# Optimization experiments

Measured on AMD Instinct MI355X. Metric: run time of the kernel, lower is better.

## Reference

```python
import jax, jax.numpy as jnp
from jax import lax
import numpy as np

B = 2; C = 128; H = 128; W = 128; NPIX = H * W
HTH = 184; HTW = 180; NBINS = HTH * HTW
NSPH = 16384; KHT = 8; KSPH = 16
N0, N1, N2 = 1024, 256, 64
K0, K1, K2 = 8, 8, 8
EPS = 1e-5


def setup_inputs() -> dict:
    key = jax.random.key(0)
    ks = jax.random.split(key, 24)
    f32 = jnp.float32
    inp = {}
    inp["image"] = jax.random.normal(ks[0], (B, C, H, W), f32)
    inp["bn_gamma"] = jnp.ones((C,), f32)
    inp["bn_beta"] = jnp.zeros((C,), f32)
    inp["ht_idx"] = jax.random.randint(ks[1], (NBINS, KHT), 0, NPIX, jnp.int32)
    inp["ht_w"] = jax.random.uniform(ks[2], (NBINS, KHT), f32)
    inp["w_htconv"] = jax.random.normal(ks[3], (3, 3, C, C), f32) / np.sqrt(9.0 * C)
    inp["htbn_gamma"] = jnp.ones((C,), f32)
    inp["htbn_beta"] = jnp.zeros((C,), f32)
    inp["sph_idx"] = jax.random.randint(ks[4], (NSPH, KSPH), 0, NBINS, jnp.int32)
    inp["sph_w"] = jax.random.uniform(ks[5], (NSPH, KSPH), f32)
    inp["w_sc"] = jax.random.normal(ks[6], (3, 64, C), f32) / np.sqrt(1.0 * C)
    inp["b_sc"] = jnp.zeros((3, 64), f32)
    inp["scbn_gamma"] = jnp.ones((3, 64), f32)
    inp["scbn_beta"] = jnp.zeros((3, 64), f32)
    inp["dgcn_w"] = jax.random.normal(ks[7], (3, 4, 128, 64), f32) / np.sqrt(128.0)
    inp["dgcn_b"] = jnp.zeros((3, 4, 64), f32)
    inp["dgcn_hw"] = jax.random.normal(ks[8], (3, 64), f32) / 8.0
    inp["dgcn_hb"] = jnp.zeros((3,), f32)
    inp["ind0"] = jax.random.randint(ks[9], (B, N0), 0, NSPH, jnp.int32)
    inp["ind1"] = jax.random.randint(ks[10], (B, 3, N1), 0, NSPH, jnp.int32)
    inp["ind2"] = jax.random.randint(ks[11], (B, 3, N2), 0, NSPH, jnp.int32)
    # kNN-style edges: structured centers (each node repeated k times), random neighbors
    c0 = jnp.tile(jnp.repeat(jnp.arange(N0, dtype=jnp.int32), K0)[None], (B, 1))
    inp["edge0"] = jnp.stack([c0, jax.random.randint(ks[12], (B, N0 * K0), 0, N0, jnp.int32)], 1)
    c1 = jnp.broadcast_to(jnp.repeat(jnp.arange(N1, dtype=jnp.int32), K1)[None, None], (B, 3, N1 * K1))
    inp["edge1"] = jnp.stack([c1, jax.random.randint(ks[13], (B, 3, N1 * K1), 0, N1, jnp.int32)], 2)
    c2 = jnp.broadcast_to(jnp.repeat(jnp.arange(N2, dtype=jnp.int32), K2)[None, None], (B, 3, N2 * K2))
    inp["edge2"] = jnp.stack([c2, jax.random.randint(ks[14], (B, 3, N2 * K2), 0, N2, jnp.int32)], 2)
    inp["target0"] = jax.random.randint(ks[15], (B, N0), 0, 2, jnp.int32)
    inp["target1"] = jax.random.randint(ks[16], (B * 3, N1), 0, 2, jnp.int32)
    inp["target2"] = jax.random.randint(ks[17], (B * 3, N2), 0, 2, jnp.int32)
    return inp


def _bn2d(x, g, b):
    m = x.mean((0, 2, 3), keepdims=True)
    v = x.var((0, 2, 3), keepdims=True)
    return g[None, :, None, None] * (x - m) * lax.rsqrt(v + EPS) + b[None, :, None, None]


def _sphere(x_htf, sph_idx, sph_w, ind):
    # x_htf: [B,C,NBINS]; ind: [B,S] -> weighted gather of HT bins per sphere node
    mi = sph_idx[ind]          # [B,S,K]
    mw = sph_w[ind]            # [B,S,K]
    g = jax.vmap(lambda xb, ib: xb[:, ib])(x_htf, mi)   # [B,C,S,K]
    return (g * mw[:, None]).sum(-1)                    # [B,C,S]


def _sconv(x, w, b, g, be):
    # 1x1 conv [B,C,S]->[B,64,S] + BN1d (batch stats) + ReLU
    y = jnp.einsum('oc,bcs->bos', w, x) + b[None, :, None]
    m = y.mean((0, 2), keepdims=True)
    v = y.var((0, 2), keepdims=True)
    return jax.nn.relu(g[None, :, None] * (y - m) * lax.rsqrt(v + EPS) + be[None, :, None])


def _dgcn(x, edge, ws, bs, hw, hb, n, k):
    # x: [Bg,n,64]; edge: [Bg,2,n*k] (row0=center, row1=neighbor); 4 EdgeConv layers
    for i in range(4):
        xc = jnp.take_along_axis(x, edge[:, 0, :, None], axis=1)   # [Bg,n*k,Cin]
        xn = jnp.take_along_axis(x, edge[:, 1, :, None], axis=1)
        h = jax.nn.relu(jnp.concatenate([xc, xn - xc], -1) @ ws[i] + bs[i])
        x = h.reshape(x.shape[0], n, k, -1).max(2)                 # max over neighbors
    return x @ hw + hb                                             # [Bg,n] logits


def _bce(logits, target):
    t = target.astype(logits.dtype)
    l = jnp.maximum(logits, 0.0) - logits * t + jnp.log1p(jnp.exp(-jnp.abs(logits)))
    pos = t > 0.5
    npos = jnp.maximum(pos.sum(), 1).astype(l.dtype)
    nneg = jnp.maximum((~pos).sum(), 1).astype(l.dtype)
    return jnp.where(pos, l, 0.0).sum() / npos, jnp.where(pos, 0.0, l).sum() / nneg


def _forward(image, bn_gamma, bn_beta, ht_idx, ht_w, w_htconv, htbn_gamma, htbn_beta,
             sph_idx, sph_w, w_sc, b_sc, scbn_gamma, scbn_beta,
             dgcn_w, dgcn_b, dgcn_hw, dgcn_hb,
             ind0, ind1, ind2, edge0, edge1, edge2, target0, target1, target2):
    x = jax.nn.relu(_bn2d(image, bn_gamma, bn_beta))
    xf = x.reshape(B, C, NPIX)
    # Hough voting: each HT bin accumulates KHT weighted pixels
    ht = (xf[:, :, ht_idx] * ht_w).sum(-1).reshape(B, C, HTH, HTW)
    hc = lax.conv_general_dilated(ht, w_htconv, (1, 1), 'SAME',
                                  dimension_numbers=('NCHW', 'HWIO', 'NCHW'))
    x_htf = jax.nn.relu(_bn2d(hc, htbn_gamma, htbn_beta)).reshape(B, C, NBINS)

    # scale 0
    x0 = _sconv(_sphere(x_htf, sph_idx, sph_w, ind0),
                w_sc[0], b_sc[0], scbn_gamma[0], scbn_beta[0]).transpose(0, 2, 1)
    x0 = _dgcn(x0, edge0, dgcn_w[0], dgcn_b[0], dgcn_hw[0], dgcn_hb[0], N0, K0)   # [B,N0]
    # scale 1 (3 vanishing-point branches folded into batch)
    x1 = _sconv(_sphere(x_htf, sph_idx, sph_w, ind1.reshape(B, -1)),
                w_sc[1], b_sc[1], scbn_gamma[1], scbn_beta[1]).transpose(0, 2, 1)
    x1 = _dgcn(x1.reshape(B * 3, N1, 64), edge1.reshape(B * 3, 2, N1 * K1),
               dgcn_w[1], dgcn_b[1], dgcn_hw[1], dgcn_hb[1], N1, K1)              # [B*3,N1]
    # scale 2
    x2 = _sconv(_sphere(x_htf, sph_idx, sph_w, ind2.reshape(B, -1)),
                w_sc[2], b_sc[2], scbn_gamma[2], scbn_beta[2]).transpose(0, 2, 1)
    x2 = _dgcn(x2.reshape(B * 3, N2, 64), edge2.reshape(B * 3, 2, N2 * K2),
               dgcn_w[2], dgcn_b[2], dgcn_hw[2], dgcn_hb[2], N2, K2)              # [B*3,N2]

    lp0, ln0 = _bce(x0, target0)
    lp1, ln1 = _bce(x1, target1)
    lp2, ln2 = _bce(x2, target2)
    losses = jnp.stack([lp0, ln0, lp1, ln1, lp2, ln2])
    preds = jnp.concatenate([jax.nn.sigmoid(x0).reshape(B, -1),
                             jax.nn.sigmoid(x1).reshape(B, -1),
                             jax.nn.sigmoid(x2).reshape(B, -1)], axis=1)
    return losses, preds


def reference(image, bn_gamma, bn_beta, ht_idx, ht_w, w_htconv, htbn_gamma, htbn_beta,
              sph_idx, sph_w, w_sc, b_sc, scbn_gamma, scbn_beta,
              dgcn_w, dgcn_b, dgcn_hw, dgcn_hb,
              ind0, ind1, ind2, edge0, edge1, edge2, target0, target1, target2):
    return _forward(image, bn_gamma, bn_beta, ht_idx, ht_w, w_htconv, htbn_gamma, htbn_beta,
                    sph_idx, sph_w, w_sc, b_sc, scbn_gamma, scbn_beta,
                    dgcn_w, dgcn_b, dgcn_hw, dgcn_hb,
                    ind0, ind1, ind2, edge0, edge1, edge2, target0, target1, target2)
```

## Files before the change

### kernel.cpp

```cpp
#include <hip/hip_runtime.h>
#include <math.h>

#define B_ 2
#define C_ 128
#define NPIX_ 16384
#define HTH_ 184
#define HTW_ 180
#define NBINS_ 33120
#define PH_ 186
#define PW_ 184
#define NPB_ 1984
#define TOTN_ 3968
#define EPS_ 1e-5f

#define ST_HC_SUM 0
#define ST_HC_SQ  128
#define ST_SC_SUM 256
#define ST_SC_SQ  448
#define ST_LOSS   640
#define ST_IMG_A  704
#define ST_IMG_D  832
#define ST_IMG_S1 1472
#define ST_IMG_S2 1600

typedef __attribute__((ext_vector_type(8))) short v8s;
typedef __attribute__((ext_vector_type(4))) float v4f;

__device__ inline unsigned short f2b(float f) {
  unsigned u = __builtin_bit_cast(unsigned, f);
  unsigned r = u + 0x7fffu + ((u >> 16) & 1u);
  return (unsigned short)(r >> 16);
}
__device__ inline float b2f(unsigned short u) {
  unsigned v = ((unsigned)u) << 16;
  return __builtin_bit_cast(float, v);
}

__global__ void kw_weights(const float* __restrict__ w, const float* __restrict__ dw,
                           unsigned short* __restrict__ wtb, unsigned short* __restrict__ dwb) {
  int i = blockIdx.x*256 + threadIdx.x;
  if (i < 147456) {
    int tap = i >> 14, z = i & 16383;
    int j = z & 7, lane = (z >> 3) & 63, nt = (z >> 9) & 7, kt = (z >> 12) & 3;
    int l = lane & 15, q = lane >> 4;
    int co = nt*16 + l, ci = kt*32 + q*8 + j;
    wtb[i] = f2b(w[(tap*C_ + ci)*C_ + co]);
  } else {
    int i2 = i - 147456;
    int sl = i2 >> 13, z = i2 & 8191;
    int j = z & 7, lane = (z >> 3) & 63, nt = (z >> 9) & 3, kt = (z >> 11) & 3;
    int l = lane & 15, q = lane >> 4;
    int co = nt*16 + l, cc = kt*32 + q*8 + j;
    dwb[i2] = f2b(dw[(sl*128 + cc)*64 + co]);
  }
}

__global__ void k1_img_stats(const float* __restrict__ img, float* __restrict__ st) {
  int c = blockIdx.x; int chunk = blockIdx.y; int tid = threadIdx.x;
  float s1 = 0.f, s2 = 0.f;
  for (int i = chunk*4096 + tid; i < (chunk+1)*4096; i += 256) {
    int b = i >> 14, p = i & (NPIX_-1);
    float v = img[((size_t)(b*C_ + c))*NPIX_ + p];
    s1 += v; s2 += v*v;
  }
  __shared__ float r1[256], r2[256];
  r1[tid] = s1; r2[tid] = s2; __syncthreads();
  for (int off = 128; off; off >>= 1) {
    if (tid < off) { r1[tid] += r1[tid+off]; r2[tid] += r2[tid+off]; }
    __syncthreads();
  }
  if (tid == 0) {
    atomicAdd(&st[ST_IMG_S1 + c], r1[0]);
    atomicAdd(&st[ST_IMG_S2 + c], r2[0]);
  }
}
__global__ void k1b_fin(const float* __restrict__ g, const float* __restrict__ be,
                        float* __restrict__ st) {
  int c = threadIdx.x;
  float n = (float)(B_*NPIX_);
  float m = st[ST_IMG_S1+c]/n;
  float var = st[ST_IMG_S2+c]/n - m*m;
  float a = g[c]*rsqrtf(var + EPS_);
  st[ST_IMG_A+c] = a; st[ST_IMG_D+c] = be[c] - a*m;
}

__global__ void k2_bnrelu_t(const float* __restrict__ img, const float* __restrict__ st,
                            unsigned short* __restrict__ xt) {
  __shared__ float tile[32*65];
  int p0 = blockIdx.x*64, c0 = blockIdx.y*32, b = blockIdx.z;
  int tid = threadIdx.x;
  for (int r = 0; r < 8; r++) {
    int flat = tid + r*256;
    int row = flat >> 6, col = flat & 63;
    int c = c0 + row;
    float v = img[((size_t)(b*C_ + c))*NPIX_ + p0 + col];
    tile[row*65 + col] = fmaxf(st[ST_IMG_A + c]*v + st[ST_IMG_D + c], 0.f);
  }
  __syncthreads();
  for (int r = 0; r < 4; r++) {
    int flat = (tid + r*256)*2;
    int pl = flat >> 5, cl = flat & 31;
    unsigned lo = f2b(tile[cl*65 + pl]);
    unsigned hi = f2b(tile[(cl+1)*65 + pl]);
    *(unsigned*)&xt[((size_t)b*NPIX_ + p0 + pl)*C_ + c0 + cl] = lo | (hi << 16);
  }
}

__global__ void k3z_border(unsigned* __restrict__ htb2) {
  int i = blockIdx.x*256 + threadIdx.x;
  int d = i & 63;
  int cell = i >> 6;
  int b = cell / 1112, j = cell % 1112;
  int y, x;
  if (j < 184) { y = 0; x = j; }
  else if (j < 368) { y = 185; x = j - 184; }
  else { int c = j - 368; int xi = c / 186; y = c % 186; x = xi == 0 ? 0 : 180 + xi; }
  htb2[((size_t)(b*PH_ + y)*PW_ + x)*64 + d] = 0u;
}

__global__ void k3_hough(const unsigned* __restrict__ xt2, const int* __restrict__ hidx,
                         const float* __restrict__ hwt, unsigned* __restrict__ htb2) {
  int tid = threadIdx.x;
  int bin = blockIdx.x*4 + (tid >> 6);
  int b = blockIdx.y;
  int lane = tid & 63;
  const unsigned* base = xt2 + (size_t)b*NPIX_*64 + lane;
  float acc0 = 0.f, acc1 = 0.f;
  #pragma unroll
  for (int k = 0; k < 8; k++) {
    int p = hidx[bin*8 + k];
    float w = hwt[bin*8 + k];
    unsigned dv = base[(size_t)p*64];
    acc0 += w * b2f((unsigned short)(dv & 0xffff));
    acc1 += w * b2f((unsigned short)(dv >> 16));
  }
  int y = bin / HTW_, x = bin - y*HTW_;
  unsigned lo = f2b(acc0), hi = f2b(acc1);
  htb2[((size_t)(b*PH_ + y + 1)*PW_ + (x+1))*64 + lane] = lo | (hi << 16);
}

__global__ __launch_bounds__(256) void k4_mfma(
    const unsigned short* __restrict__ htb, const unsigned short* __restrict__ wtb,
    unsigned short* __restrict__ hcb, float* __restrict__ st) {
  __shared__ float red[1152];
  int tid = threadIdx.x;
  int w = tid >> 6, lane = tid & 63;
  int quad = lane >> 4, l16 = lane & 15;
  int ph = w & 1, ch = w >> 1;
  int b = blockIdx.y;
  int p0 = blockIdx.x*128 + ph*64;
  size_t ab[4];
  #pragma unroll
  for (int t = 0; t < 4; t++) {
    int px = p0 + t*16 + l16; if (px > NBINS_-1) px = NBINS_-1;
    int y = px / HTW_, x = px % HTW_;
    ab[t] = (((size_t)(b*PH_ + y))*PW_ + x)*C_ + quad*8;
  }
  v4f acc[4][4];
  #pragma unroll
  for (int t = 0; t < 4; t++)
    #pragma unroll
    for (int nt = 0; nt < 4; nt++) acc[t][nt] = (v4f){0,0,0,0};

  const v8s* wbase = (const v8s*)wtb + lane;
  #pragma unroll
  for (int tap = 0; tap < 9; tap++) {
    int dy = tap/3, dx = tap - dy*3;
    int toff = (dy*PW_ + dx)*C_;
    #pragma unroll
    for (int kt = 0; kt < 4; kt++) {
      v8s a[4];
      #pragma unroll
      for (int t = 0; t < 4; t++) a[t] = *(const v8s*)&htb[ab[t] + toff + kt*32];
      #pragma unroll
      for (int nt = 0; nt < 4; nt++) {
        v8s bf = wbase[(((tap*4 + kt)*8) + ch*4 + nt)*64];
        #pragma unroll
        for (int t = 0; t < 4; t++)
          acc[t][nt] = __builtin_amdgcn_mfma_f32_16x16x32_bf16(a[t], bf, acc[t][nt], 0, 0, 0);
      }
    }
  }
  float s1[4] = {0,0,0,0}, s2[4] = {0,0,0,0};
  #pragma unroll
  for (int t = 0; t < 4; t++) {
    #pragma unroll
    for (int nt = 0; nt < 4; nt++) {
      int co = ch*64 + nt*16 + l16;
      #pragma unroll
      for (int reg = 0; reg < 4; reg++) {
        int po = p0 + t*16 + quad*4 + reg;
        if (po < NBINS_) {
          float v = acc[t][nt][reg];
          hcb[((size_t)b*NBINS_ + po)*C_ + co] = f2b(v);
          s1[nt] += v; s2[nt] += v*v;
        }
      }
    }
  }
  int slot = ph*4 + quad;
  #pragma unroll
  for (int nt = 0; nt < 4; nt++) red[(ch*64 + nt*16 + l16)*9 + slot] = s1[nt];
  __syncthreads();
  if (tid < 128) {
    float s = 0.f;
    #pragma unroll
    for (int k = 0; k < 8; k++) s += red[tid*9 + k];
    atomicAdd(&st[ST_HC_SUM + tid], s);
  }
  __syncthreads();
  #pragma unroll
  for (int nt = 0; nt < 4; nt++) red[(ch*64 + nt*16 + l16)*9 + slot] = s2[nt];
  __syncthreads();
  if (tid < 128) {
    float s = 0.f;
    #pragma unroll
    for (int k = 0; k < 8; k++) s += red[tid*9 + k];
    atomicAdd(&st[ST_HC_SQ + tid], s);
  }
}

__global__ void k6_sphere(const unsigned* __restrict__ hcb2, const float* __restrict__ st,
                          const float* __restrict__ g, const float* __restrict__ be,
                          const int* __restrict__ sph_idx, const float* __restrict__ sph_w,
                          const int* __restrict__ ind0, const int* __restrict__ ind1,
                          const int* __restrict__ ind2, float* __restrict__ out) {
  int tid = threadIdx.x;
  int gn = blockIdx.x*4 + (tid >> 6);
  int lane = tid & 63;
  int b = gn / NPB_, nb = gn % NPB_;
  int v;
  if (nb < 1024) v = ind0[b*1024 + nb];
  else if (nb < 1792) v = ind1[b*768 + nb - 1024];
  else v = ind2[b*192 + nb - 1792];
  int c0 = lane*2, c1 = c0 + 1;
  float n = (float)(B_*NBINS_);
  float m0 = st[ST_HC_SUM + c0]/n, m1 = st[ST_HC_SUM + c1]/n;
  float va0 = st[ST_HC_SQ + c0]/n - m0*m0, va1 = st[ST_HC_SQ + c1]/n - m1*m1;
  float a0 = g[c0]*rsqrtf(va0 + EPS_), a1 = g[c1]*rsqrtf(va1 + EPS_);
  float d0 = be[c0] - a0*m0, d1 = be[c1] - a1*m1;
  const unsigned* base = hcb2 + (size_t)b*NBINS_*64 + lane;
  float acc0 = 0.f, acc1 = 0.f;
  #pragma unroll
  for (int k = 0; k < 16; k++) {
    int mi = sph_idx[v*16 + k];
    float mw = sph_w[v*16 + k];
    unsigned dv = base[(size_t)mi*64];
    acc0 += mw * fmaxf(a0*b2f((unsigned short)(dv & 0xffff)) + d0, 0.f);
    acc1 += mw * fmaxf(a1*b2f((unsigned short)(dv >> 16)) + d1, 0.f);
  }
  *(float2*)&out[(size_t)gn*C_ + c0] = make_float2(acc0, acc1);
}

__global__ __launch_bounds__(256) void k7_sconv(
    const float* __restrict__ xin, const float* __restrict__ w_sc,
    const float* __restrict__ b_sc, float* __restrict__ y, float* __restrict__ st) {
  __shared__ float xs[32*128];
  __shared__ float wT[128*65];
  __shared__ float red[256];
  int tid = threadIdx.x;
  int gn0 = blockIdx.x * 32;
  int nb = gn0 % NPB_;
  int s = nb < 1024 ? 0 : (nb < 1792 ? 1 : 2);
  for (int r = 0; r < 16; r++) {
    int flat = tid + r*256;
    xs[flat] = xin[(size_t)gn0*C_ + flat];
  }
  for (int r = 0; r < 32; r++) {
    int flat = tid + r*256;
    int o = flat >> 7, cc = flat & 127;
    wT[cc*65 + o] = w_sc[(s*64 + o)*C_ + cc];
  }
  __syncthreads();
  int o = tid & 63, nl = tid >> 6;
  float bias = b_sc[s*64 + o];
  float acc[8];
  #pragma unroll
  for (int i = 0; i < 8; i++) acc[i] = bias;
  for (int cc = 0; cc < 128; cc++) {
    float wv = wT[cc*65 + o];
    #pragma unroll
    for (int i = 0; i < 8; i++)
      acc[i] += xs[(nl*8 + i)*128 + cc] * wv;
  }
  float s1 = 0.f, s2 = 0.f;
  #pragma unroll
  for (int i = 0; i < 8; i++) {
    y[(size_t)(gn0 + nl*8 + i)*64 + o] = acc[i];
    s1 += acc[i]; s2 += acc[i]*acc[i];
  }
  red[tid] = s1; __syncthreads();
  if (nl == 0) atomicAdd(&st[ST_SC_SUM + s*64 + o], red[o] + red[64+o] + red[128+o] + red[192+o]);
  __syncthreads();
  red[tid] = s2; __syncthreads();
  if (nl == 0) atomicAdd(&st[ST_SC_SQ + s*64 + o], red[o] + red[64+o] + red[128+o] + red[192+o]);
}

__global__ __launch_bounds__(256) void k10_dgcn(
    const void* __restrict__ xin_, unsigned short* __restrict__ xout,
    const int* __restrict__ edge0, const int* __restrict__ edge1, const int* __restrict__ edge2,
    const unsigned short* __restrict__ dwb, const float* __restrict__ db,
    const float* __restrict__ st, const float* __restrict__ scg, const float* __restrict__ scb,
    int layer, int usebn) {
  __shared__ unsigned short E[128*136];
  __shared__ float ash[64], dsh[64];
  int tid = threadIdx.x;
  int bid = blockIdx.x;
  int s, node_base, le_blk, span; const int* ec;
  if (bid < 128) {
    s = 0; int b = bid >> 6; node_base = b*NPB_; le_blk = (bid & 63)*128;
    span = 8192; ec = edge0 + b*2*8192;
  } else if (bid < 224) {
    int j = bid - 128; s = 1; int seg = j >> 4; int b = seg/3, vp = seg%3;
    node_base = b*NPB_ + 1024 + vp*256; le_blk = (j & 15)*128;
    span = 2048; ec = edge1 + ((b*3+vp)*2)*2048;
  } else {
    int j = bid - 224; s = 2; int seg = j >> 2; int b = seg/3, vp = seg%3;
    node_base = b*NPB_ + 1792 + vp*64; le_blk = (j & 3)*128;
    span = 512; ec = edge2 + ((b*3+vp)*2)*512;
  }
  const int* en = ec + span;
  if (usebn) {
    if (tid < 64) {
      float n = s==0 ? 2048.f : (s==1 ? 1536.f : 384.f);
      float m = st[ST_SC_SUM + s*64 + tid]/n;
      float var = st[ST_SC_SQ + s*64 + tid]/n - m*m;
      float a = scg[s*64 + tid]*rsqrtf(var + EPS_);
      ash[tid] = a; dsh[tid] = scb[s*64 + tid] - a*m;
    }
    __syncthreads();
  }
  {
    int r = tid >> 1, h = tid & 1;
    int e = le_blk + r;
    int ci = ec[e], ni = en[e];
    if (usebn) {
      const float* xc = (const float*)xin_ + (size_t)(node_base + ci)*64;
      const float* xn = (const float*)xin_ + (size_t)(node_base + ni)*64;
      #pragma unroll
      for (int c8 = 0; c8 < 64; c8 += 8) {
        v8s pk;
        #pragma unroll
        for (int j = 0; j < 8; j++) {
          int c = c8 + j;
          float vc = fmaxf(ash[c]*xc[c] + dsh[c], 0.f);
          float val = vc;
          if (h) val = fmaxf(ash[c]*xn[c] + dsh[c], 0.f) - vc;
          pk[j] = (short)f2b(val);
        }
        *(v8s*)&E[r*136 + h*64 + c8] = pk;
      }
    } else {
      const unsigned short* xc = (const unsigned short*)xin_ + (size_t)(node_base + ci)*64;
      const unsigned short* xn = (const unsigned short*)xin_ + (size_t)(node_base + ni)*64;
      #pragma unroll
      for (int c8 = 0; c8 < 64; c8 += 8) {
        v8s vc8 = *(const v8s*)&xc[c8];
        v8s pk = vc8;
        if (h) {
          v8s vn8 = *(const v8s*)&xn[c8];
          #pragma unroll
          for (int j = 0; j < 8; j++)
            pk[j] = (short)f2b(b2f((unsigned short)vn8[j]) - b2f((unsigned short)vc8[j]));
        }
        *(v8s*)&E[r*136 + h*64 + c8] = pk;
      }
    }
  }
  __syncthreads();
  int wave = tid >> 6, lane = tid & 63;
  int quad = lane >> 4, l16 = lane & 15;
  const unsigned short* wb = dwb + (size_t)(s*4 + layer)*8192;
  v4f acc[2][4];
  #pragma unroll
  for (int t = 0; t < 2; t++)
    #pragma unroll
    for (int nt = 0; nt < 4; nt++) acc[t][nt] = (v4f){0,0,0,0};
  #pragma unroll
  for (int kt = 0; kt < 4; kt++) {
    v8s a0 = *(const v8s*)&E[(wave*32 + l16)*136 + quad*8 + kt*32];
    v8s a1 = *(const v8s*)&E[(wave*32 + 16 + l16)*136 + quad*8 + kt*32];
    #pragma unroll
    for (int nt = 0; nt < 4; nt++) {
      v8s bf = *(const v8s*)&wb[((kt*4 + nt)*64 + lane)*8];
      acc[0][nt] = __builtin_amdgcn_mfma_f32_16x16x32_bf16(a0, bf, acc[0][nt], 0, 0, 0);
      acc[1][nt] = __builtin_amdgcn_mfma_f32_16x16x32_bf16(a1, bf, acc[1][nt], 0, 0, 0);
    }
  }
  int vb0 = le_blk/8 + wave*4;
  #pragma unroll
  for (int t = 0; t < 2; t++) {
    #pragma unroll
    for (int nt = 0; nt < 4; nt++) {
      float bias = db[(s*4 + layer)*64 + nt*16 + l16];
      float m = fmaxf(fmaxf(acc[t][nt][0], acc[t][nt][1]),
                      fmaxf(acc[t][nt][2], acc[t][nt][3]));
      m = fmaxf(m + bias, 0.f);
      float other = __shfl_xor(m, 16);
      m = fmaxf(m, other);
      if ((quad & 1) == 0) {
        int v = vb0 + t*2 + (quad >> 1);
        xout[(size_t)(node_base + v)*64 + nt*16 + l16] = f2b(m);
      }
    }
  }
}

__global__ __launch_bounds__(256) void k11_head(
    const unsigned short* __restrict__ x, const float* __restrict__ hw, const float* __restrict__ hb,
    const int* __restrict__ t0, const int* __restrict__ t1, const int* __restrict__ t2,
    float* __restrict__ out, float* __restrict__ st) {
  __shared__ float shw[192];
  int tid = threadIdx.x;
  if (tid < 192) shw[tid] = hw[tid];
  __syncthreads();
  int gn = blockIdx.x*256 + tid;
  bool valid = gn < TOTN_;
  int g = valid ? gn : TOTN_-1;
  int b = g / NPB_, nb = g % NPB_;
  int s, tg;
  if (nb < 1024) { s = 0; tg = t0[b*1024 + nb]; }
  else if (nb < 1792) { s = 1; int j = nb-1024; tg = t1[(b*3 + (j>>8))*256 + (j&255)]; }
  else { s = 2; int j = nb-1792; tg = t2[(b*3 + (j>>6))*64 + (j&63)]; }
  const unsigned short* row = x + (size_t)g*64;
  float logit = hb[s];
  #pragma unroll
  for (int c8 = 0; c8 < 64; c8 += 8) {
    v8s v = *(const v8s*)&row[c8];
    #pragma unroll
    for (int j = 0; j < 8; j++)
      logit += b2f((unsigned short)v[j]) * shw[s*64 + c8 + j];
  }
  if (valid) out[6 + gn] = 1.f / (1.f + expf(-logit));
  float tf = (float)tg;
  float l = fmaxf(logit, 0.f) - logit*tf + log1pf(expf(-fabsf(logit)));
  float sp = (valid && tg) ? l : 0.f;
  float sn = (valid && !tg) ? l : 0.f;
  float cp = (valid && tg) ? 1.f : 0.f;
  float cn = (valid && !tg) ? 1.f : 0.f;
  for (int off = 32; off; off >>= 1) {
    sp += __shfl_down(sp, off);
    sn += __shfl_down(sn, off);
    cp += __shfl_down(cp, off);
    cn += __shfl_down(cn, off);
  }
  if ((tid & 63) == 0) {
    atomicAdd(&st[ST_LOSS + s*4 + 0], sp);
    atomicAdd(&st[ST_LOSS + s*4 + 1], sn);
    atomicAdd(&st[ST_LOSS + s*4 + 2], cp);
    atomicAdd(&st[ST_LOSS + s*4 + 3], cn);
  }
}

__global__ void k12_fin(const float* __restrict__ st, float* __restrict__ out) {
  int i = threadIdx.x;
  if (i < 6) {
    int s = i >> 1; int pos = !(i & 1);
    float sum = st[ST_LOSS + s*4 + (pos ? 0 : 1)];
    float cnt = st[ST_LOSS + s*4 + (pos ? 2 : 3)];
    out[i] = sum / fmaxf(cnt, 1.f);
  }
}

extern "C" void kernel_launch(void* const* d_in, const int* in_sizes, int n_in,
                              void* d_out, int out_size, void* d_ws, size_t ws_size,
                              hipStream_t stream) {
  const float* image  = (const float*)d_in[0];
  const float* bn_g   = (const float*)d_in[1];
  const float* bn_b   = (const float*)d_in[2];
  const int*   ht_idx = (const int*)  d_in[3];
  const float* ht_w   = (const float*)d_in[4];
  const float* w_conv = (const float*)d_in[5];
  const float* htbn_g = (const float*)d_in[6];
  const float* htbn_b = (const float*)d_in[7];
  const int*   sph_idx= (const int*)  d_in[8];
  const float* sph_w  = (const float*)d_in[9];
  const float* w_sc   = (const float*)d_in[10];
  const float* b_sc   = (const float*)d_in[11];
  const float* scbn_g = (const float*)d_in[12];
  const float* scbn_b = (const float*)d_in[13];
  const float* dgcn_w = (const float*)d_in[14];
  const float* dgcn_b = (const float*)d_in[15];
  const float* dgcn_hw= (const float*)d_in[16];
  const float* dgcn_hb= (const float*)d_in[17];
  const int*   ind0   = (const int*)  d_in[18];
  const int*   ind1   = (const int*)  d_in[19];
  const int*   ind2   = (const int*)  d_in[20];
  const int*   edge0  = (const int*)  d_in[21];
  const int*   edge1  = (const int*)  d_in[22];
  const int*   edge2  = (const int*)  d_in[23];
  const int*   t0     = (const int*)  d_in[24];
  const int*   t1     = (const int*)  d_in[25];
  const int*   t2     = (const int*)  d_in[26];
  float* out = (float*)d_out;

  char* ws = (char*)d_ws;
  unsigned short* x_t   = (unsigned short*)(ws);
  unsigned short* htb   = (unsigned short*)(ws +  8388608);
  unsigned short* hcb   = (unsigned short*)(ws + 25911296);
  unsigned short* wtb   = (unsigned short*)(ws + 42868736);
  unsigned short* dwb   = (unsigned short*)(ws + 43163648);
  float*          sph_o = (float*)(ws + 43360256);
  float*          y_sc  = (float*)(ws + 45391872);
  unsigned short* xdgA  = (unsigned short*)(ws + 46407680);
  unsigned short* xdgB  = (unsigned short*)(ws + 46915584);
  float*          st    = (float*)(ws + 47423488);

  hipMemsetAsync(st, 0, 1728*sizeof(float), stream);
  kw_weights<<<960, 256, 0, stream>>>(w_conv, dgcn_w, wtb, dwb);
  k3z_border<<<556, 256, 0, stream>>>((unsigned*)htb);
  k1_img_stats<<<dim3(128,8), 256, 0, stream>>>(image, st);
  k1b_fin<<<1, 128, 0, stream>>>(bn_g, bn_b, st);
  k2_bnrelu_t<<<dim3(256,4,2), 256, 0, stream>>>(image, st, x_t);
  k3_hough<<<dim3(NBINS_/4, B_), 256, 0, stream>>>((const unsigned*)x_t, ht_idx, ht_w, (unsigned*)htb);
  k4_mfma<<<dim3(259, 2), 256, 0, stream>>>(htb, wtb, hcb, st);
  k6_sphere<<<TOTN_/4, 256, 0, stream>>>((const unsigned*)hcb, st, htbn_g, htbn_b, sph_idx, sph_w, ind0, ind1, ind2, sph_o);
  k7_sconv<<<TOTN_/32, 256, 0, stream>>>(sph_o, w_sc, b_sc, y_sc, st);
  k10_dgcn<<<248, 256, 0, stream>>>((const void*)y_sc, xdgA, edge0, edge1, edge2, dwb, dgcn_b, st, scbn_g, scbn_b, 0, 1);
  k10_dgcn<<<248, 256, 0, stream>>>((const void*)xdgA, xdgB, edge0, edge1, edge2, dwb, dgcn_b, st, scbn_g, scbn_b, 1, 0);
  k10_dgcn<<<248, 256, 0, stream>>>((const void*)xdgB, xdgA, edge0, edge1, edge2, dwb, dgcn_b, st, scbn_g, scbn_b, 2, 0);
  k10_dgcn<<<248, 256, 0, stream>>>((const void*)xdgA, xdgB, edge0, edge1, edge2, dwb, dgcn_b, st, scbn_g, scbn_b, 3, 0);
  k11_head<<<16, 256, 0, stream>>>(xdgB, dgcn_hw, dgcn_hb, t0, t1, t2, out, st);
  k12_fin<<<1, 64, 0, stream>>>(st, out);
}
```

Baseline: 277.9 us.

## Stage Hough-conv tiles in LDS and fuse small setup kernels

```diff
diff --git a/kernel.cpp b/kernel.cpp
--- a/kernel.cpp
+++ b/kernel.cpp
@@ -18,8 +18,6 @@
 #define ST_SC_SUM 256
 #define ST_SC_SQ  448
 #define ST_LOSS   640
-#define ST_IMG_A  704
-#define ST_IMG_D  832
 #define ST_IMG_S1 1472
 #define ST_IMG_S2 1600
 
@@ -36,22 +34,33 @@
   return __builtin_bit_cast(float, v);
 }
 
-__global__ void kw_weights(const float* __restrict__ w, const float* __restrict__ dw,
-                           unsigned short* __restrict__ wtb, unsigned short* __restrict__ dwb) {
-  int i = blockIdx.x*256 + threadIdx.x;
-  if (i < 147456) {
-    int tap = i >> 14, z = i & 16383;
+__global__ void kprep(const float* __restrict__ w, const float* __restrict__ dw,
+                      unsigned short* __restrict__ wtb, unsigned short* __restrict__ dwb,
+                      unsigned* __restrict__ htb2) {
+  int idx = blockIdx.x*256 + threadIdx.x;
+  if (idx < 147456) {
+    int tap = idx >> 14, z = idx & 16383;
     int j = z & 7, lane = (z >> 3) & 63, nt = (z >> 9) & 7, kt = (z >> 12) & 3;
     int l = lane & 15, q = lane >> 4;
     int co = nt*16 + l, ci = kt*32 + q*8 + j;
-    wtb[i] = f2b(w[(tap*C_ + ci)*C_ + co]);
-  } else {
-    int i2 = i - 147456;
+    wtb[idx] = f2b(w[(tap*C_ + ci)*C_ + co]);
+  } else if (idx < 245760) {
+    int i2 = idx - 147456;
     int sl = i2 >> 13, z = i2 & 8191;
     int j = z & 7, lane = (z >> 3) & 63, nt = (z >> 9) & 3, kt = (z >> 11) & 3;
     int l = lane & 15, q = lane >> 4;
     int co = nt*16 + l, cc = kt*32 + q*8 + j;
     dwb[i2] = f2b(dw[(sl*128 + cc)*64 + co]);
+  } else {
+    int i = idx - 245760;
+    int d = i & 63;
+    int cell = i >> 6;
+    int b = cell / 1112, j = cell % 1112;
+    int y, x;
+    if (j < 184) { y = 0; x = j; }
+    else if (j < 368) { y = 185; x = j - 184; }
+    else { int c = j - 368; int xi = c / 186; y = c % 186; x = xi == 0 ? 0 : 180 + xi; }
+    htb2[((size_t)(b*PH_ + y)*PW_ + x)*64 + d] = 0u;
   }
 }
 
@@ -74,27 +83,28 @@
     atomicAdd(&st[ST_IMG_S2 + c], r2[0]);
   }
 }
-__global__ void k1b_fin(const float* __restrict__ g, const float* __restrict__ be,
-                        float* __restrict__ st) {
-  int c = threadIdx.x;
-  float n = (float)(B_*NPIX_);
-  float m = st[ST_IMG_S1+c]/n;
-  float var = st[ST_IMG_S2+c]/n - m*m;
-  float a = g[c]*rsqrtf(var + EPS_);
-  st[ST_IMG_A+c] = a; st[ST_IMG_D+c] = be[c] - a*m;
-}
 
 __global__ void k2_bnrelu_t(const float* __restrict__ img, const float* __restrict__ st,
+                            const float* __restrict__ g, const float* __restrict__ be,
                             unsigned short* __restrict__ xt) {
   __shared__ float tile[32*65];
+  __shared__ float ash[32], dsh[32];
   int p0 = blockIdx.x*64, c0 = blockIdx.y*32, b = blockIdx.z;
   int tid = threadIdx.x;
+  if (tid < 32) {
+    int c = c0 + tid;
+    float n = (float)(B_*NPIX_);
+    float m = st[ST_IMG_S1+c]/n;
+    float var = st[ST_IMG_S2+c]/n - m*m;
+    float a = g[c]*rsqrtf(var + EPS_);
+    ash[tid] = a; dsh[tid] = be[c] - a*m;
+  }
+  __syncthreads();
   for (int r = 0; r < 8; r++) {
     int flat = tid + r*256;
     int row = flat >> 6, col = flat & 63;
-    int c = c0 + row;
-    float v = img[((size_t)(b*C_ + c))*NPIX_ + p0 + col];
-    tile[row*65 + col] = fmaxf(st[ST_IMG_A + c]*v + st[ST_IMG_D + c], 0.f);
+    float v = img[((size_t)(b*C_ + c0 + row))*NPIX_ + p0 + col];
+    tile[row*65 + col] = fmaxf(ash[row]*v + dsh[row], 0.f);
   }
   __syncthreads();
   for (int r = 0; r < 4; r++) {
@@ -106,22 +116,11 @@
   }
 }
 
-__global__ void k3z_border(unsigned* __restrict__ htb2) {
-  int i = blockIdx.x*256 + threadIdx.x;
-  int d = i & 63;
-  int cell = i >> 6;
-  int b = cell / 1112, j = cell % 1112;
-  int y, x;
-  if (j < 184) { y = 0; x = j; }
-  else if (j < 368) { y = 185; x = j - 184; }
-  else { int c = j - 368; int xi = c / 186; y = c % 186; x = xi == 0 ? 0 : 180 + xi; }
-  htb2[((size_t)(b*PH_ + y)*PW_ + x)*64 + d] = 0u;
-}
-
 __global__ void k3_hough(const unsigned* __restrict__ xt2, const int* __restrict__ hidx,
                          const float* __restrict__ hwt, unsigned* __restrict__ htb2) {
   int tid = threadIdx.x;
-  int bin = blockIdx.x*4 + (tid >> 6);
+  int wv = __builtin_amdgcn_readfirstlane(tid >> 6);
+  int bin = blockIdx.x*4 + wv;
   int b = blockIdx.y;
   int lane = tid & 63;
   const unsigned* base = xt2 + (size_t)b*NPIX_*64 + lane;
@@ -139,48 +138,66 @@
   htb2[((size_t)(b*PH_ + y + 1)*PW_ + (x+1))*64 + lane] = lo | (hi << 16);
 }
 
-__global__ __launch_bounds__(256) void k4_mfma(
+__global__ __launch_bounds__(256, 4) void k4_mfma(
     const unsigned short* __restrict__ htb, const unsigned short* __restrict__ wtb,
     unsigned short* __restrict__ hcb, float* __restrict__ st) {
-  __shared__ float red[1152];
+  __shared__ char smem[33792];
   int tid = threadIdx.x;
   int w = tid >> 6, lane = tid & 63;
   int quad = lane >> 4, l16 = lane & 15;
   int ph = w & 1, ch = w >> 1;
-  int b = blockIdx.y;
-  int p0 = blockIdx.x*128 + ph*64;
-  size_t ab[4];
-  #pragma unroll
-  for (int t = 0; t < 4; t++) {
-    int px = p0 + t*16 + l16; if (px > NBINS_-1) px = NBINS_-1;
-    int y = px / HTW_, x = px % HTW_;
-    ab[t] = (((size_t)(b*PH_ + y))*PW_ + x)*C_ + quad*8;
-  }
+  int b = blockIdx.z;
+  int x0 = blockIdx.x*64;
+  int y0 = blockIdx.y*2;
+  const v8s* wbase = (const v8s*)wtb + lane;
   v4f acc[4][4];
   #pragma unroll
   for (int t = 0; t < 4; t++)
     #pragma unroll
     for (int nt = 0; nt < 4; nt++) acc[t][nt] = (v4f){0,0,0,0};
 
-  const v8s* wbase = (const v8s*)wtb + lane;
-  #pragma unroll
-  for (int tap = 0; tap < 9; tap++) {
-    int dy = tap/3, dx = tap - dy*3;
-    int toff = (dy*PW_ + dx)*C_;
-    #pragma unroll
-    for (int kt = 0; kt < 4; kt++) {
-      v8s a[4];
+  for (int half = 0; half < 2; half++) {
+    __syncthreads();
+    #pragma unroll
+    for (int it = 0; it < 9; it++) {
+      int c = tid + it*256;
+      if (c < 2112) {
+        int px = c >> 3, part = c & 7;
+        int r = px/66, xc = px - r*66;
+        int gx = x0 + xc; if (gx > PW_-1) gx = PW_-1;
+        const uint4* gp = (const uint4*)(htb + (((size_t)(b*PH_ + y0 + r))*PW_ + gx)*C_ + half*64) + part;
+        *(uint4*)(smem + px*128 + ((part ^ (xc & 7)) << 4)) = *gp;
+      }
+    }
+    __syncthreads();
+    #pragma unroll
+    for (int dy = 0; dy < 3; dy++) {
       #pragma unroll
-      for (int t = 0; t < 4; t++) a[t] = *(const v8s*)&htb[ab[t] + toff + kt*32];
-      #pragma unroll
-      for (int nt = 0; nt < 4; nt++) {
-        v8s bf = wbase[(((tap*4 + kt)*8) + ch*4 + nt)*64];
+      for (int dx = 0; dx < 3; dx++) {
+        int sw = ((l16 + dx) & 7) << 4;
+        int rowbase = ((ph + dy)*66 + l16 + dx)*128;
         #pragma unroll
-        for (int t = 0; t < 4; t++)
-          acc[t][nt] = __builtin_amdgcn_mfma_f32_16x16x32_bf16(a[t], bf, acc[t][nt], 0, 0, 0);
+        for (int kt2 = 0; kt2 < 2; kt2++) {
+          int qo = quad*16 + kt2*64;
+          v8s a[4];
+          #pragma unroll
+          for (int t = 0; t < 4; t++)
+            a[t] = *(const v8s*)(smem + rowbase + t*2048 + (qo ^ sw));
+          int kt = half*2 + kt2;
+          #pragma unroll
+          for (int nt = 0; nt < 4; nt++) {
+            v8s bf = wbase[(((dy*3 + dx)*4 + kt)*8 + ch*4 + nt)*64];
+            #pragma unroll
+            for (int t = 0; t < 4; t++)
+              acc[t][nt] = __builtin_amdgcn_mfma_f32_16x16x32_bf16(a[t], bf, acc[t][nt], 0, 0, 0);
+          }
+        }
       }
     }
   }
+  __syncthreads();
+  float* red = (float*)smem;
+  int y = y0 + ph;
   float s1[4] = {0,0,0,0}, s2[4] = {0,0,0,0};
   #pragma unroll
   for (int t = 0; t < 4; t++) {
@@ -189,10 +206,10 @@
       int co = ch*64 + nt*16 + l16;
       #pragma unroll
       for (int reg = 0; reg < 4; reg++) {
-        int po = p0 + t*16 + quad*4 + reg;
-        if (po < NBINS_) {
+        int x = x0 + t*16 + quad*4 + reg;
+        if (x < HTW_) {
           float v = acc[t][nt][reg];
-          hcb[((size_t)b*NBINS_ + po)*C_ + co] = f2b(v);
+          hcb[((size_t)b*NBINS_ + y*HTW_ + x)*C_ + co] = f2b(v);
           s1[nt] += v; s2[nt] += v*v;
         }
       }
@@ -226,7 +243,8 @@
                           const int* __restrict__ ind0, const int* __restrict__ ind1,
                           const int* __restrict__ ind2, float* __restrict__ out) {
   int tid = threadIdx.x;
-  int gn = blockIdx.x*4 + (tid >> 6);
+  int wv = __builtin_amdgcn_readfirstlane(tid >> 6);
+  int gn = blockIdx.x*4 + wv;
   int lane = tid & 63;
   int b = gn / NPB_, nb = gn % NPB_;
   int v;
@@ -507,13 +525,11 @@
   float*          st    = (float*)(ws + 47423488);
 
   hipMemsetAsync(st, 0, 1728*sizeof(float), stream);
-  kw_weights<<<960, 256, 0, stream>>>(w_conv, dgcn_w, wtb, dwb);
-  k3z_border<<<556, 256, 0, stream>>>((unsigned*)htb);
+  kprep<<<1516, 256, 0, stream>>>(w_conv, dgcn_w, wtb, dwb, (unsigned*)htb);
   k1_img_stats<<<dim3(128,8), 256, 0, stream>>>(image, st);
-  k1b_fin<<<1, 128, 0, stream>>>(bn_g, bn_b, st);
-  k2_bnrelu_t<<<dim3(256,4,2), 256, 0, stream>>>(image, st, x_t);
+  k2_bnrelu_t<<<dim3(256,4,2), 256, 0, stream>>>(image, st, bn_g, bn_b, x_t);
   k3_hough<<<dim3(NBINS_/4, B_), 256, 0, stream>>>((const unsigned*)x_t, ht_idx, ht_w, (unsigned*)htb);
-  k4_mfma<<<dim3(259, 2), 256, 0, stream>>>(htb, wtb, hcb, st);
+  k4_mfma<<<dim3(3, 92, 2), 256, 0, stream>>>(htb, wtb, hcb, st);
   k6_sphere<<<TOTN_/4, 256, 0, stream>>>((const unsigned*)hcb, st, htbn_g, htbn_b, sph_idx, sph_w, ind0, ind1, ind2, sph_o);
   k7_sconv<<<TOTN_/32, 256, 0, stream>>>(sph_o, w_sc, b_sc, y_sc, st);
   k10_dgcn<<<248, 256, 0, stream>>>((const void*)y_sc, xdgA, edge0, edge1, edge2, dwb, dgcn_b, st, scbn_g, scbn_b, 0, 1);
```

Result: faster. 267.8 us (-3.6%).
